# Kernel tuning notes

Hardware: AMD Instinct MI355X
Metric: run time of the kernel (lower is better)

Reference implementation:

```python
import jax, jax.numpy as jnp
import numpy as np

EPS = 1e-8


def setup_inputs() -> dict:
    key = jax.random.key(0)
    ks = jax.random.split(key, 7)
    S, B, E, D, A = 2048, 32, 1024, 1024, 1024
    return {
        "decoder_state": jax.random.normal(ks[0], (B, D), jnp.float32),
        "encoder_states": jax.random.normal(ks[1], (S, B, E), jnp.float32),
        "noise": jax.random.normal(ks[2], (S, B), jnp.float32),
        "W_dec": jax.random.normal(ks[3], (D, A), jnp.float32) * (D ** -0.5),
        "W_enc": jax.random.normal(ks[4], (E, A), jnp.float32) * (E ** -0.5),
        "b": jax.random.normal(ks[5], (A,), jnp.float32) * 0.02,
        "v": jax.random.normal(ks[6], (A,), jnp.float32) * (A ** -0.5),
    }


def reference(decoder_state, encoder_states, noise, W_dec, W_enc, b, v):
    S, B, E = encoder_states.shape
    # Additive (Bahdanau) monotonic energy: e_sb = v . tanh(W_d s + W_e h + b)
    dec_proj = decoder_state @ W_dec                         # [B, A]
    enc_proj = jnp.einsum("sbe,ea->sba", encoder_states, W_enc)  # [S, B, A]
    energy = jnp.einsum("sba,a->sb", jnp.tanh(enc_proj + dec_proj[None] + b), v)
    # p_choose with pre-sigmoid Gaussian noise (noise_avg=0, noise_var=1)
    p_choose = jax.nn.sigmoid(energy + noise)                # [S, B]

    # previous_attention is None -> one-hot at source position 0
    prev_attn = jnp.zeros((S, B), p_choose.dtype).at[0].set(1.0)

    # exclusive cumprod of (1 - p) along src dim
    cp = jnp.cumprod(1.0 - p_choose, axis=0)
    cumprod_one_minus_p = jnp.concatenate(
        [jnp.ones((1, B), p_choose.dtype), cp[:-1]], axis=0)
    denom = jnp.clip(cumprod_one_minus_p, EPS, 1.0)
    alpha = p_choose * cumprod_one_minus_p * jnp.cumsum(prev_attn / denom, axis=0)

    # mass preservation (no padding mask): dump residual mass on last frame
    residual = 1.0 - jnp.clip(jnp.sum(alpha[:-1], axis=0), 0.0, 1.0)
    alpha = alpha.at[-1].set(residual)

    beta = alpha  # hard monotonic attention: beta == alpha
    weighted_context = jnp.einsum("sbe,sb->be", encoder_states, beta)  # [B, E]
    return weighted_context, alpha
```

## Files before the change

kernel.cpp:

```cpp
#include <hip/hip_runtime.h>
#include <hip/hip_fp16.h>

#define S_DIM 2048
#define B_DIM 32
#define E_DIM 1024
#define A_DIM 1024
#define D_DIM 1024
#define M_DIM (S_DIM * B_DIM)

typedef _Float16 f16x8 __attribute__((ext_vector_type(8)));
typedef _Float16 f16x4 __attribute__((ext_vector_type(4)));
typedef float f32x4 __attribute__((ext_vector_type(4)));

#define OFF_ENC 0ull
#define OFF_WT  134217728ull
#define OFF_DP  (OFF_WT + 2097152ull)
#define OFF_EN  (OFF_DP + 131072ull)

__device__ inline void load_lds16(const void* g, void* l) {
    __builtin_amdgcn_global_load_lds((const __attribute__((address_space(1))) void*)g,
                                     (__attribute__((address_space(3))) void*)l, 16, 0, 0);
}

__global__ void convert_enc_kernel(const float4* __restrict__ in, f16x4* __restrict__ out) {
    int idx = blockIdx.x * 256 + threadIdx.x;
    float4 f = in[idx];
    f16x4 o = { (_Float16)f.x, (_Float16)f.y, (_Float16)f.z, (_Float16)f.w };
    out[idx] = o;
}

__global__ void transpose_wenc_kernel(const float* __restrict__ W, _Float16* __restrict__ WT) {
    __shared__ _Float16 tile[32][33];
    int a0 = blockIdx.x * 32, e0 = blockIdx.y * 32;
    int tx = threadIdx.x & 31, ty = threadIdx.x >> 5;
    #pragma unroll
    for (int i = 0; i < 32; i += 8)
        tile[ty + i][tx] = (_Float16)W[(size_t)(e0 + ty + i) * A_DIM + a0 + tx];
    __syncthreads();
    #pragma unroll
    for (int i = 0; i < 32; i += 8)
        WT[(size_t)(a0 + ty + i) * E_DIM + e0 + tx] = tile[tx][ty + i];
}

__global__ void decproj_kernel(const float* __restrict__ dec, const float* __restrict__ Wd,
                               const float* __restrict__ bias, float* __restrict__ dp) {
    int a = blockIdx.x * 256 + threadIdx.x;
    int b = blockIdx.y;
    float acc = bias[a];
    const float* dr = dec + (size_t)b * D_DIM;
    const float* wcol = Wd + a;
    #pragma unroll 8
    for (int d = 0; d < D_DIM; ++d)
        acc += dr[d] * wcol[(size_t)d * A_DIM];
    dp[(size_t)b * A_DIM + a] = acc;
}

__global__ __launch_bounds__(256, 2)
void energy_gemm_kernel(const _Float16* __restrict__ Af, const _Float16* __restrict__ Bt,
                        const float* __restrict__ dp, const float* __restrict__ v,
                        float* __restrict__ energy) {
    __shared__ alignas(16) _Float16 Atile[128 * 32];
    __shared__ alignas(16) _Float16 Btile[128 * 32];

    const int tid = threadIdx.x;
    const int wid = tid >> 6;
    const int lane = tid & 63;
    const int quad = lane >> 4;
    const int l15 = lane & 15;

    const int bid = blockIdx.x + (int)(gridDim.x * blockIdx.y);
    const int xcd = bid & 7;
    const int local = bid >> 3;
    const int m0 = (xcd * 64 + (local >> 3)) * 128;
    const int n0 = (local & 7) * 128;

    const int wm = (wid & 1) * 64;
    const int wn = (wid >> 1) * 64;

    const int srow = wid * 16 + (lane >> 2);
    const int skel = (((lane & 3) ^ ((lane >> 3) & 3)) * 8);
    const _Float16* Ag0 = Af + (size_t)(m0 + srow) * E_DIM + skel;
    const _Float16* Ag1 = Af + (size_t)(m0 + 64 + srow) * E_DIM + skel;
    const _Float16* Bg0 = Bt + (size_t)(n0 + srow) * E_DIM + skel;
    const _Float16* Bg1 = Bt + (size_t)(n0 + 64 + srow) * E_DIM + skel;
    _Float16* Al0 = Atile + wid * 512;
    _Float16* Al1 = Atile + 2048 + wid * 512;
    _Float16* Bl0 = Btile + wid * 512;
    _Float16* Bl1 = Btile + 2048 + wid * 512;

    const int swz = (quad ^ ((l15 >> 1) & 3)) * 8;

    f32x4 acc[4][4] = {};

    for (int k0 = 0; k0 < E_DIM; k0 += 32) {
        __syncthreads();
        load_lds16(Ag0 + k0, Al0);
        load_lds16(Ag1 + k0, Al1);
        load_lds16(Bg0 + k0, Bl0);
        load_lds16(Bg1 + k0, Bl1);
        __syncthreads();

        f16x8 af[4], bfr[4];
        #pragma unroll
        for (int i = 0; i < 4; ++i)
            af[i] = *(const f16x8*)&Atile[(wm + i * 16 + l15) * 32 + swz];
        #pragma unroll
        for (int j = 0; j < 4; ++j)
            bfr[j] = *(const f16x8*)&Btile[(wn + j * 16 + l15) * 32 + swz];
        #pragma unroll
        for (int i = 0; i < 4; ++i)
            #pragma unroll
            for (int j = 0; j < 4; ++j)
                acc[i][j] = __builtin_amdgcn_mfma_f32_16x16x32_f16(af[i], bfr[j], acc[i][j], 0, 0, 0);
    }

    float vf[4];
    #pragma unroll
    for (int j = 0; j < 4; ++j) vf[j] = v[n0 + wn + j * 16 + l15];

    #pragma unroll
    for (int i = 0; i < 4; ++i) {
        #pragma unroll
        for (int r = 0; r < 4; ++r) {
            int m = m0 + wm + i * 16 + quad * 4 + r;
            int bidx = m & 31;
            float sum = 0.f;
            #pragma unroll
            for (int j = 0; j < 4; ++j) {
                int a = n0 + wn + j * 16 + l15;
                float x = acc[i][j][r] + dp[bidx * A_DIM + a];
                float ex = __expf(2.f * x);
                float t = 1.f - 2.f * __builtin_amdgcn_rcpf(ex + 1.f);
                sum += t * vf[j];
            }
            sum += __shfl_xor(sum, 1);
            sum += __shfl_xor(sum, 2);
            sum += __shfl_xor(sum, 4);
            sum += __shfl_xor(sum, 8);
            if (l15 == 0) atomicAdd(&energy[bidx * S_DIM + (m >> 5)], sum);
        }
    }
}

__global__ void scan_alpha_kernel(const float* __restrict__ energy, const float* __restrict__ noise,
                                  float* __restrict__ alpha) {
    __shared__ float sc[256];
    __shared__ float red[256];
    const int b = blockIdx.x;
    const int t = threadIdx.x;
    float p[8], q[8];
    float prod = 1.f;
    #pragma unroll
    for (int k = 0; k < 8; ++k) {
        int s = t * 8 + k;
        float x = energy[b * S_DIM + s] + noise[s * B_DIM + b];
        p[k] = __builtin_amdgcn_rcpf(1.f + __expf(-x));
        q[k] = __builtin_amdgcn_rcpf(1.f + __expf(x));
        prod *= q[k];
    }
    sc[t] = prod;
    __syncthreads();
    for (int off = 1; off < 256; off <<= 1) {
        float mine = sc[t];
        float other = (t >= off) ? sc[t - off] : 1.f;
        __syncthreads();
        sc[t] = mine * other;
        __syncthreads();
    }
    float run = (t > 0) ? sc[t - 1] : 1.f;
    float lsum = 0.f;
    #pragma unroll
    for (int k = 0; k < 8; ++k) {
        int s = t * 8 + k;
        float al = p[k] * run;
        run *= q[k];
        if (s < S_DIM - 1) { alpha[s * B_DIM + b] = al; lsum += al; }
    }
    red[t] = lsum;
    __syncthreads();
    for (int off = 128; off > 0; off >>= 1) {
        if (t < off) red[t] += red[t + off];
        __syncthreads();
    }
    if (t == 0) {
        float tot = fminf(fmaxf(red[0], 0.f), 1.f);
        alpha[(S_DIM - 1) * B_DIM + b] = 1.f - tot;
    }
}

__global__ void wc_kernel(const _Float16* __restrict__ enc, const float* __restrict__ alpha,
                          float* __restrict__ wc) {
    __shared__ float red[128][8];
    const int b = blockIdx.y;
    const int t = threadIdx.x;
    const int e0 = (t & 127) * 8;
    const int half = t >> 7;
    int s = blockIdx.x * 128 + half;
    float acc[8] = {};
    for (int i = 0; i < 64; ++i, s += 2) {
        float al = alpha[s * B_DIM + b];
        f16x8 r = *(const f16x8*)&enc[((size_t)s * B_DIM + b) * E_DIM + e0];
        #pragma unroll
        for (int k = 0; k < 8; ++k) acc[k] += al * (float)r[k];
    }
    if (half) {
        #pragma unroll
        for (int k = 0; k < 8; ++k) red[t - 128][k] = acc[k];
    }
    __syncthreads();
    if (!half) {
        #pragma unroll
        for (int k = 0; k < 8; ++k)
            atomicAdd(&wc[b * E_DIM + e0 + k], acc[k] + red[t][k]);
    }
}

extern "C" void kernel_launch(void* const* d_in, const int* in_sizes, int n_in,
                              void* d_out, int out_size, void* d_ws, size_t ws_size,
                              hipStream_t stream) {
    const float* dec   = (const float*)d_in[0];
    const float* enc   = (const float*)d_in[1];
    const float* noise = (const float*)d_in[2];
    const float* Wd    = (const float*)d_in[3];
    const float* We    = (const float*)d_in[4];
    const float* bias  = (const float*)d_in[5];
    const float* v     = (const float*)d_in[6];

    char* ws = (char*)d_ws;
    _Float16* encf = (_Float16*)(ws + OFF_ENC);
    _Float16* wtf  = (_Float16*)(ws + OFF_WT);
    float* dp      = (float*)(ws + OFF_DP);
    float* energy  = (float*)(ws + OFF_EN);

    float* wc    = (float*)d_out;
    float* alpha = (float*)d_out + B_DIM * E_DIM;

    (void)hipMemsetAsync(wc, 0, B_DIM * E_DIM * sizeof(float), stream);
    (void)hipMemsetAsync(energy, 0, M_DIM * sizeof(float), stream);

    convert_enc_kernel<<<dim3(M_DIM * E_DIM / 4 / 256), 256, 0, stream>>>((const float4*)enc, (f16x4*)encf);
    transpose_wenc_kernel<<<dim3(32, 32), 256, 0, stream>>>(We, wtf);
    decproj_kernel<<<dim3(4, 32), 256, 0, stream>>>(dec, Wd, bias, dp);
    energy_gemm_kernel<<<dim3(8, 512), 256, 0, stream>>>(encf, wtf, dp, v, energy);
    scan_alpha_kernel<<<dim3(32), 256, 0, stream>>>(energy, noise, alpha);
    wc_kernel<<<dim3(16, 32), 256, 0, stream>>>(encf, alpha, wc);
}
```

Before: 665.3 us.

## Enlarge energy GEMM tiles to 256x256x64 with double-buffered async LDS loads

The energy GEMM now uses 512-thread blocks computing 256x256 output tiles with a K step of 64, in place of 128x128 tiles with a K step of 32. LDS is double-buffered, and global-to-LDS loads for stage t+2 are issued while stage t is being computed, synchronised with explicit vmcnt waits and barriers. MFMA sections are wrapped in setprio. This is meant to raise arithmetic intensity and hide memory latency behind the matrix work. The cost is 128KB of LDS per block, which limits occupancy, plus higher register pressure from 32 accumulators per thread.

```diff
diff --git a/kernel.cpp b/kernel.cpp
--- a/kernel.cpp
+++ b/kernel.cpp
@@ -55,71 +55,100 @@
     dp[(size_t)b * A_DIM + a] = acc;
 }
 
-__global__ __launch_bounds__(256, 2)
+__global__ __launch_bounds__(512, 2)
 void energy_gemm_kernel(const _Float16* __restrict__ Af, const _Float16* __restrict__ Bt,
                         const float* __restrict__ dp, const float* __restrict__ v,
                         float* __restrict__ energy) {
-    __shared__ alignas(16) _Float16 Atile[128 * 32];
-    __shared__ alignas(16) _Float16 Btile[128 * 32];
+    __shared__ alignas(16) _Float16 Atile[2][256 * 64];
+    __shared__ alignas(16) _Float16 Btile[2][256 * 64];
 
     const int tid = threadIdx.x;
     const int wid = tid >> 6;
     const int lane = tid & 63;
     const int quad = lane >> 4;
     const int l15 = lane & 15;
-
-    const int bid = blockIdx.x + (int)(gridDim.x * blockIdx.y);
+    const int l7 = l15 & 7;
+
+    const int bid = blockIdx.x;
     const int xcd = bid & 7;
     const int local = bid >> 3;
-    const int m0 = (xcd * 64 + (local >> 3)) * 128;
-    const int n0 = (local & 7) * 128;
-
-    const int wm = (wid & 1) * 64;
-    const int wn = (wid >> 1) * 64;
-
-    const int srow = wid * 16 + (lane >> 2);
-    const int skel = (((lane & 3) ^ ((lane >> 3) & 3)) * 8);
-    const _Float16* Ag0 = Af + (size_t)(m0 + srow) * E_DIM + skel;
-    const _Float16* Ag1 = Af + (size_t)(m0 + 64 + srow) * E_DIM + skel;
-    const _Float16* Bg0 = Bt + (size_t)(n0 + srow) * E_DIM + skel;
-    const _Float16* Bg1 = Bt + (size_t)(n0 + 64 + srow) * E_DIM + skel;
-    _Float16* Al0 = Atile + wid * 512;
-    _Float16* Al1 = Atile + 2048 + wid * 512;
-    _Float16* Bl0 = Btile + wid * 512;
-    _Float16* Bl1 = Btile + 2048 + wid * 512;
-
-    const int swz = (quad ^ ((l15 >> 1) & 3)) * 8;
-
-    f32x4 acc[4][4] = {};
-
-    for (int k0 = 0; k0 < E_DIM; k0 += 32) {
-        __syncthreads();
-        load_lds16(Ag0 + k0, Al0);
-        load_lds16(Ag1 + k0, Al1);
-        load_lds16(Bg0 + k0, Bl0);
-        load_lds16(Bg1 + k0, Bl1);
-        __syncthreads();
-
-        f16x8 af[4], bfr[4];
-        #pragma unroll
-        for (int i = 0; i < 4; ++i)
-            af[i] = *(const f16x8*)&Atile[(wm + i * 16 + l15) * 32 + swz];
-        #pragma unroll
-        for (int j = 0; j < 4; ++j)
-            bfr[j] = *(const f16x8*)&Btile[(wn + j * 16 + l15) * 32 + swz];
-        #pragma unroll
-        for (int i = 0; i < 4; ++i)
+    const int m0 = (xcd * 32 + (local >> 2)) * 256;
+    const int n0 = (local & 3) * 256;
+
+    const int wm = (wid >> 2) * 128;
+    const int wn = (wid & 3) * 64;
+
+    const int lr = lane >> 3;
+    const int lcol = ((lane & 7) ^ lr) * 8;
+    const int srow = wid * 8;
+    const _Float16* Ag = Af + (size_t)(m0 + srow + lr) * E_DIM + lcol;
+    const _Float16* Bg = Bt + (size_t)(n0 + srow + lr) * E_DIM + lcol;
+
+#define STAGE(bufi, k0)                                                       \
+    {                                                                         \
+        _Float16* ad = &Atile[bufi][srow * 64];                               \
+        _Float16* bd = &Btile[bufi][srow * 64];                               \
+        _Pragma("unroll")                                                     \
+        for (int p = 0; p < 4; ++p) {                                         \
+            load_lds16(Ag + (size_t)p * 64 * E_DIM + (k0), ad + p * 4096);    \
+            load_lds16(Bg + (size_t)p * 64 * E_DIM + (k0), bd + p * 4096);    \
+        }                                                                     \
+    }
+
+    f32x4 acc[8][4] = {};
+
+    STAGE(0, 0)
+    STAGE(1, 64)
+
+    for (int t = 0; t < 16; ++t) {
+        const int buf = t & 1;
+        if (t == 15) asm volatile("s_waitcnt vmcnt(0)" ::: "memory");
+        else         asm volatile("s_waitcnt vmcnt(8)" ::: "memory");
+        __builtin_amdgcn_s_barrier();
+        asm volatile("" ::: "memory");
+
+        #pragma unroll
+        for (int kh = 0; kh < 2; ++kh) {
+            f16x8 bf[4];
             #pragma unroll
-            for (int j = 0; j < 4; ++j)
-                acc[i][j] = __builtin_amdgcn_mfma_f32_16x16x32_f16(af[i], bfr[j], acc[i][j], 0, 0, 0);
-    }
+            for (int j = 0; j < 4; ++j) {
+                const int row = wn + j * 16 + l15;
+                const int slot = (quad + kh * 4) ^ l7;
+                bf[j] = *(const f16x8*)&Btile[buf][row * 64 + slot * 8];
+            }
+            #pragma unroll
+            for (int mh = 0; mh < 2; ++mh) {
+                f16x8 af[4];
+                #pragma unroll
+                for (int i = 0; i < 4; ++i) {
+                    const int row = wm + mh * 64 + i * 16 + l15;
+                    const int slot = (quad + kh * 4) ^ l7;
+                    af[i] = *(const f16x8*)&Atile[buf][row * 64 + slot * 8];
+                }
+                __builtin_amdgcn_s_setprio(1);
+                #pragma unroll
+                for (int i = 0; i < 4; ++i)
+                    #pragma unroll
+                    for (int j = 0; j < 4; ++j)
+                        acc[mh * 4 + i][j] = __builtin_amdgcn_mfma_f32_16x16x32_f16(
+                            af[i], bf[j], acc[mh * 4 + i][j], 0, 0, 0);
+                __builtin_amdgcn_s_setprio(0);
+            }
+        }
+
+        asm volatile("" ::: "memory");
+        __builtin_amdgcn_s_barrier();
+        asm volatile("" ::: "memory");
+        if (t + 2 < 16) STAGE(buf, (t + 2) * 64)
+    }
+#undef STAGE
 
     float vf[4];
     #pragma unroll
     for (int j = 0; j < 4; ++j) vf[j] = v[n0 + wn + j * 16 + l15];
 
     #pragma unroll
-    for (int i = 0; i < 4; ++i) {
+    for (int i = 0; i < 8; ++i) {
         #pragma unroll
         for (int r = 0; r < 4; ++r) {
             int m = m0 + wm + i * 16 + quad * 4 + r;
@@ -130,8 +159,8 @@
                 int a = n0 + wn + j * 16 + l15;
                 float x = acc[i][j][r] + dp[bidx * A_DIM + a];
                 float ex = __expf(2.f * x);
-                float t = 1.f - 2.f * __builtin_amdgcn_rcpf(ex + 1.f);
-                sum += t * vf[j];
+                float th = 1.f - 2.f * __builtin_amdgcn_rcpf(ex + 1.f);
+                sum += th * vf[j];
             }
             sum += __shfl_xor(sum, 1);
             sum += __shfl_xor(sum, 2);
@@ -241,7 +270,7 @@
     convert_enc_kernel<<<dim3(M_DIM * E_DIM / 4 / 256), 256, 0, stream>>>((const float4*)enc, (f16x4*)encf);
     transpose_wenc_kernel<<<dim3(32, 32), 256, 0, stream>>>(We, wtf);
     decproj_kernel<<<dim3(4, 32), 256, 0, stream>>>(dec, Wd, bias, dp);
-    energy_gemm_kernel<<<dim3(8, 512), 256, 0, stream>>>(encf, wtf, dp, v, energy);
+    energy_gemm_kernel<<<dim3(1024), 512, 0, stream>>>(encf, wtf, dp, v, energy);
     scan_alpha_kernel<<<dim3(32), 256, 0, stream>>>(energy, noise, alpha);
     wc_kernel<<<dim3(16, 32), 256, 0, stream>>>(encf, alpha, wc);
 }
```

After: 678.9 us. 2.0% more time.
